# Kernel optimization log

Hardware: AMD Instinct MI355X
Metric: run time of the kernel (lower is better)

The kernel has to match this reference:

```python
import jax, jax.numpy as jnp
import numpy as np

PREF_DIM = 2
PREF_EMB = 64
HIDDEN = 512
NUM_CHUNKS = 105
CHUNK_EMB = 64
NUM_WS = 11
W_DIM = 20000


def setup_inputs() -> dict:
    key = jax.random.key(0)
    ks = jax.random.split(key, 12)
    in_dim = PREF_EMB + CHUNK_EMB
    inp = {
        "preference": jax.random.uniform(ks[0], (PREF_DIM,), dtype=jnp.float32),
        "pref_emb": 0.1 * jax.random.normal(ks[1], (PREF_DIM, PREF_EMB), dtype=jnp.float32),
        "chunk_emb": 0.1 * jax.random.normal(ks[2], (NUM_CHUNKS, CHUNK_EMB), dtype=jnp.float32),
        "W1": jax.random.normal(ks[3], (HIDDEN, in_dim), dtype=jnp.float32) / np.sqrt(in_dim),
        "b1": jnp.zeros((HIDDEN,), dtype=jnp.float32),
        "W2": jax.random.normal(ks[4], (HIDDEN, HIDDEN), dtype=jnp.float32) / np.sqrt(HIDDEN),
        "b2": jnp.zeros((HIDDEN,), dtype=jnp.float32),
        "W3": jax.random.normal(ks[5], (HIDDEN, HIDDEN), dtype=jnp.float32) / np.sqrt(HIDDEN),
        "b3": jnp.zeros((HIDDEN,), dtype=jnp.float32),
        "ws": 0.1 * jax.random.normal(ks[6], (NUM_WS, W_DIM, HIDDEN), dtype=jnp.float32),
    }
    return inp


def reference(preference, pref_emb, chunk_emb, W1, b1, W2, b2, W3, b3, ws):
    # pref_embedding = sum_i preference[i] * pref_emb[i]  -> [PREF_EMB]
    pref_embedding = preference @ pref_emb
    # Batch all chunks: concat(pref_embedding, chunk_emb[c]) -> [C, PREF_EMB+CHUNK_EMB]
    C = chunk_emb.shape[0]
    x = jnp.concatenate(
        [jnp.broadcast_to(pref_embedding, (C, pref_embedding.shape[0])), chunk_emb],
        axis=1,
    )
    # 3-layer MLP (Linear/ReLU/Linear/ReLU/Linear)
    h = jax.nn.relu(x @ W1.T + b1)
    h = jax.nn.relu(h @ W2.T + b2)
    rep = h @ W3.T + b3  # [C, HIDDEN]
    # Per chunk, concat over ws of F.linear(rep, w): [C, NUM_WS, W_DIM]
    out = jnp.einsum("ch,kwh->ckw", rep, ws)
    # Flat weight vector (original then reshapes contiguous slices into a dict;
    # that slicing is a pure view op on this vector)
    return out.reshape(-1)
```

## Files before the change

kernel.cpp:

```cpp
#include <hip/hip_runtime.h>


typedef __bf16 bf16x8 __attribute__((ext_vector_type(8)));
typedef float f32x4 __attribute__((ext_vector_type(4)));

#define NUM_CHUNKS 105
#define HIDDEN 512
#define N_COLS 220000
#define PAD_CHUNKS 112
#define REP_CHUNKS 7168

__global__ void mlp_kernel(const float* __restrict__ pref,
                           const float* __restrict__ pref_emb,
                           const float* __restrict__ chunk_emb,
                           const float* __restrict__ W1, const float* __restrict__ b1,
                           const float* __restrict__ W2, const float* __restrict__ b2,
                           const float* __restrict__ W3, const float* __restrict__ b3,
                           __bf16* __restrict__ repf) {
  __shared__ float x[128];
  __shared__ float h1[512];
  __shared__ float h2[512];
  const int tid = threadIdx.x;
  const int c = blockIdx.x;
  const int t = c >> 4, mmc = c & 15;

  if (c >= NUM_CHUNKS) {
    for (int jj = tid; jj < 512; jj += 256) {
      const int ss = jj >> 5, qq = (jj >> 3) & 3, j = jj & 7;
      const long idx = (((long)(ss * 7 + t) * 4 + qq) * 16 + mmc) * 8 + j;
      repf[idx] = (__bf16)0.f;
    }
    return;
  }

  if (tid < 64) {
    x[tid] = pref[0] * pref_emb[tid] + pref[1] * pref_emb[64 + tid];
  } else if (tid < 128) {
    x[tid] = chunk_emb[c * 64 + (tid - 64)];
  }
  __syncthreads();

  for (int jj = tid; jj < 512; jj += 256) {
    float s = b1[jj];
    const f32x4* wr = (const f32x4*)(W1 + jj * 128);
#pragma unroll
    for (int i = 0; i < 32; ++i) {
      f32x4 w = wr[i];
      s += w[0] * x[i * 4 + 0] + w[1] * x[i * 4 + 1] +
           w[2] * x[i * 4 + 2] + w[3] * x[i * 4 + 3];
    }
    h1[jj] = fmaxf(s, 0.f);
  }
  __syncthreads();

  for (int jj = tid; jj < 512; jj += 256) {
    float s = b2[jj];
    const f32x4* wr = (const f32x4*)(W2 + jj * 512);
#pragma unroll 8
    for (int i = 0; i < 128; ++i) {
      f32x4 w = wr[i];
      s += w[0] * h1[i * 4 + 0] + w[1] * h1[i * 4 + 1] +
           w[2] * h1[i * 4 + 2] + w[3] * h1[i * 4 + 3];
    }
    h2[jj] = fmaxf(s, 0.f);
  }
  __syncthreads();

  for (int jj = tid; jj < 512; jj += 256) {
    float s = b3[jj];
    const f32x4* wr = (const f32x4*)(W3 + jj * 512);
#pragma unroll 8
    for (int i = 0; i < 128; ++i) {
      f32x4 w = wr[i];
      s += w[0] * h2[i * 4 + 0] + w[1] * h2[i * 4 + 1] +
           w[2] * h2[i * 4 + 2] + w[3] * h2[i * 4 + 3];
    }
    const int ss = jj >> 5, qq = (jj >> 3) & 3, j = jj & 7;
    const long idx = (((long)(ss * 7 + t) * 4 + qq) * 16 + mmc) * 8 + j;
    repf[idx] = (__bf16)s;
  }
}

__global__ __launch_bounds__(256, 1) void gemm_ws(
    const float* __restrict__ ws,
    const bf16x8* __restrict__ repf,
    float* __restrict__ out) {
  __shared__ bf16x8 Alds[REP_CHUNKS];

  const int tid = threadIdx.x;
  const int lane = tid & 63;
  const int wv = tid >> 6;
  const int q = lane >> 4;
  const int mm = lane & 15;

#pragma unroll
  for (int i = 0; i < 28; ++i) {
    const bf16x8* g = repf + wv * 1792 + i * 64 + lane;
    __builtin_amdgcn_global_load_lds(
        (const __attribute__((address_space(1))) unsigned int*)g,
        (__attribute__((address_space(3))) unsigned int*)&Alds[wv * 1792 + i * 64],
        16, 0, 0);
  }

  const long cb = (long)blockIdx.x * 128 + wv * 32;
  const long col0 = cb + mm;
  const long col1 = col0 + 16;
  const bool v0 = col0 < N_COLS;
  const bool v1 = col1 < N_COLS;
  const long cl0 = v0 ? col0 : 0;
  const long cl1 = v1 ? col1 : 0;
  const f32x4* w0 = (const f32x4*)(ws + cl0 * 512) + q * 2;
  const f32x4* w1 = (const f32x4*)(ws + cl1 * 512) + q * 2;

  f32x4 X0[3], X1[3], Y0[3], Y1[3];
#pragma unroll
  for (int p = 0; p < 3; ++p) {
    X0[p] = __builtin_nontemporal_load(w0 + p * 8);
    X1[p] = __builtin_nontemporal_load(w0 + p * 8 + 1);
    Y0[p] = __builtin_nontemporal_load(w1 + p * 8);
    Y1[p] = __builtin_nontemporal_load(w1 + p * 8 + 1);
  }

  __syncthreads();

  f32x4 acc0[7], acc1[7];
#pragma unroll
  for (int t = 0; t < 7; ++t) {
    acc0[t] = (f32x4){0.f, 0.f, 0.f, 0.f};
    acc1[t] = (f32x4){0.f, 0.f, 0.f, 0.f};
  }

  bf16x8 Aa[7], Ab[7];
#pragma unroll
  for (int t = 0; t < 7; ++t) Aa[t] = Alds[t * 64 + lane];

#pragma unroll
  for (int s = 0; s < 16; ++s) {
    if (s < 15) {
#pragma unroll
      for (int t = 0; t < 7; ++t) {
        if (s & 1) Aa[t] = Alds[(s + 1) * 448 + t * 64 + lane];
        else       Ab[t] = Alds[(s + 1) * 448 + t * 64 + lane];
      }
    }
    const int slot = s % 3;
    f32x4 x0 = X0[slot], x1 = X1[slot], y0 = Y0[slot], y1 = Y1[slot];
    bf16x8 b0, b1;
#pragma unroll
    for (int j = 0; j < 4; ++j) {
      b0[j] = (__bf16)x0[j];
      b0[4 + j] = (__bf16)x1[j];
      b1[j] = (__bf16)y0[j];
      b1[4 + j] = (__bf16)y1[j];
    }
#pragma unroll
    for (int t = 0; t < 7; ++t) {
      bf16x8 a = (s & 1) ? Ab[t] : Aa[t];
      acc0[t] = __builtin_amdgcn_mfma_f32_16x16x32_bf16(a, b0, acc0[t], 0, 0, 0);
      acc1[t] = __builtin_amdgcn_mfma_f32_16x16x32_bf16(a, b1, acc1[t], 0, 0, 0);
    }
    if (s < 13) {
      X0[slot] = __builtin_nontemporal_load(w0 + (s + 3) * 8);
      X1[slot] = __builtin_nontemporal_load(w0 + (s + 3) * 8 + 1);
      Y0[slot] = __builtin_nontemporal_load(w1 + (s + 3) * 8);
      Y1[slot] = __builtin_nontemporal_load(w1 + (s + 3) * 8 + 1);
    }
  }

#pragma unroll
  for (int t = 0; t < 7; ++t) {
    const int mbase = t * 16 + q * 4;
#pragma unroll
    for (int r = 0; r < 4; ++r) {
      const int m = mbase + r;
      if (m < NUM_CHUNKS) {
        if (v0) __builtin_nontemporal_store(acc0[t][r], out + (long)m * N_COLS + col0);
        if (v1) __builtin_nontemporal_store(acc1[t][r], out + (long)m * N_COLS + col1);
      }
    }
  }
}

extern "C" void kernel_launch(void* const* d_in, const int* in_sizes, int n_in,
                              void* d_out, int out_size, void* d_ws, size_t ws_size,
                              hipStream_t stream) {
  const float* pref      = (const float*)d_in[0];
  const float* pref_emb  = (const float*)d_in[1];
  const float* chunk_emb = (const float*)d_in[2];
  const float* W1 = (const float*)d_in[3];
  const float* b1 = (const float*)d_in[4];
  const float* W2 = (const float*)d_in[5];
  const float* b2 = (const float*)d_in[6];
  const float* W3 = (const float*)d_in[7];
  const float* b3 = (const float*)d_in[8];
  const float* ws = (const float*)d_in[9];
  float* out = (float*)d_out;
  __bf16* repf = (__bf16*)d_ws;

  mlp_kernel<<<PAD_CHUNKS, 256, 0, stream>>>(pref, pref_emb, chunk_emb,
                                             W1, b1, W2, b2, W3, b3, repf);
  const int nblk = (N_COLS + 127) / 128;
  gemm_ws<<<nblk, 256, 0, stream>>>(ws, (const bf16x8*)d_ws, out);
}
```

Before: 719.6 us.

## Make ws GEMM persistent with cross-tile prefetch; widen MLP blocks to 512 threads

The ws GEMM becomes a persistent kernel of 256 blocks that loop over column tiles. The A operand is loaded into LDS once per block, and the first weight slices of the next tile are prefetched while the current tile finishes, with the prefetch depth raised from 3 to 4 stages. The MLP kernel runs with 512 threads so each thread computes one output, and it splits each dot product across four partial sums for more ILP. The goal is to amortise the LDS staging and launch tail and keep memory streaming across tiles. The risk is lower occupancy per CU and load imbalance across tiles.

```diff
diff --git a/kernel.cpp b/kernel.cpp
--- a/kernel.cpp
+++ b/kernel.cpp
@@ -9,6 +9,8 @@
 #define N_COLS 220000
 #define PAD_CHUNKS 112
 #define REP_CHUNKS 7168
+#define N_TILES 1719
+#define GEMM_BLOCKS 256
 
 __global__ void mlp_kernel(const float* __restrict__ pref,
                            const float* __restrict__ pref_emb,
@@ -23,13 +25,12 @@
   const int tid = threadIdx.x;
   const int c = blockIdx.x;
   const int t = c >> 4, mmc = c & 15;
+  const int jj = tid;
+  const int ss = jj >> 5, qq = (jj >> 3) & 3, j = jj & 7;
+  const long fidx = (((long)(ss * 7 + t) * 4 + qq) * 16 + mmc) * 8 + j;
 
   if (c >= NUM_CHUNKS) {
-    for (int jj = tid; jj < 512; jj += 256) {
-      const int ss = jj >> 5, qq = (jj >> 3) & 3, j = jj & 7;
-      const long idx = (((long)(ss * 7 + t) * 4 + qq) * 16 + mmc) * 8 + j;
-      repf[idx] = (__bf16)0.f;
-    }
+    repf[fidx] = (__bf16)0.f;
     return;
   }
 
@@ -40,44 +41,48 @@
   }
   __syncthreads();
 
-  for (int jj = tid; jj < 512; jj += 256) {
-    float s = b1[jj];
+  {
     const f32x4* wr = (const f32x4*)(W1 + jj * 128);
-#pragma unroll
-    for (int i = 0; i < 32; ++i) {
-      f32x4 w = wr[i];
-      s += w[0] * x[i * 4 + 0] + w[1] * x[i * 4 + 1] +
-           w[2] * x[i * 4 + 2] + w[3] * x[i * 4 + 3];
-    }
-    h1[jj] = fmaxf(s, 0.f);
-  }
-  __syncthreads();
-
-  for (int jj = tid; jj < 512; jj += 256) {
-    float s = b2[jj];
+    float p0 = 0.f, p1 = 0.f, p2 = 0.f, p3 = 0.f;
+#pragma unroll
+    for (int i = 0; i < 32; i += 4) {
+      f32x4 wa = wr[i], wb = wr[i + 1], wc = wr[i + 2], wd = wr[i + 3];
+      p0 += wa[0] * x[i * 4 + 0] + wa[1] * x[i * 4 + 1] + wa[2] * x[i * 4 + 2] + wa[3] * x[i * 4 + 3];
+      p1 += wb[0] * x[i * 4 + 4] + wb[1] * x[i * 4 + 5] + wb[2] * x[i * 4 + 6] + wb[3] * x[i * 4 + 7];
+      p2 += wc[0] * x[i * 4 + 8] + wc[1] * x[i * 4 + 9] + wc[2] * x[i * 4 + 10] + wc[3] * x[i * 4 + 11];
+      p3 += wd[0] * x[i * 4 + 12] + wd[1] * x[i * 4 + 13] + wd[2] * x[i * 4 + 14] + wd[3] * x[i * 4 + 15];
+    }
+    h1[jj] = fmaxf((p0 + p1) + (p2 + p3) + b1[jj], 0.f);
+  }
+  __syncthreads();
+
+  {
     const f32x4* wr = (const f32x4*)(W2 + jj * 512);
+    float p0 = 0.f, p1 = 0.f, p2 = 0.f, p3 = 0.f;
 #pragma unroll 8
-    for (int i = 0; i < 128; ++i) {
-      f32x4 w = wr[i];
-      s += w[0] * h1[i * 4 + 0] + w[1] * h1[i * 4 + 1] +
-           w[2] * h1[i * 4 + 2] + w[3] * h1[i * 4 + 3];
-    }
-    h2[jj] = fmaxf(s, 0.f);
-  }
-  __syncthreads();
-
-  for (int jj = tid; jj < 512; jj += 256) {
-    float s = b3[jj];
+    for (int i = 0; i < 128; i += 4) {
+      f32x4 wa = wr[i], wb = wr[i + 1], wc = wr[i + 2], wd = wr[i + 3];
+      p0 += wa[0] * h1[i * 4 + 0] + wa[1] * h1[i * 4 + 1] + wa[2] * h1[i * 4 + 2] + wa[3] * h1[i * 4 + 3];
+      p1 += wb[0] * h1[i * 4 + 4] + wb[1] * h1[i * 4 + 5] + wb[2] * h1[i * 4 + 6] + wb[3] * h1[i * 4 + 7];
+      p2 += wc[0] * h1[i * 4 + 8] + wc[1] * h1[i * 4 + 9] + wc[2] * h1[i * 4 + 10] + wc[3] * h1[i * 4 + 11];
+      p3 += wd[0] * h1[i * 4 + 12] + wd[1] * h1[i * 4 + 13] + wd[2] * h1[i * 4 + 14] + wd[3] * h1[i * 4 + 15];
+    }
+    h2[jj] = fmaxf((p0 + p1) + (p2 + p3) + b2[jj], 0.f);
+  }
+  __syncthreads();
+
+  {
     const f32x4* wr = (const f32x4*)(W3 + jj * 512);
+    float p0 = 0.f, p1 = 0.f, p2 = 0.f, p3 = 0.f;
 #pragma unroll 8
-    for (int i = 0; i < 128; ++i) {
-      f32x4 w = wr[i];
-      s += w[0] * h2[i * 4 + 0] + w[1] * h2[i * 4 + 1] +
-           w[2] * h2[i * 4 + 2] + w[3] * h2[i * 4 + 3];
-    }
-    const int ss = jj >> 5, qq = (jj >> 3) & 3, j = jj & 7;
-    const long idx = (((long)(ss * 7 + t) * 4 + qq) * 16 + mmc) * 8 + j;
-    repf[idx] = (__bf16)s;
+    for (int i = 0; i < 128; i += 4) {
+      f32x4 wa = wr[i], wb = wr[i + 1], wc = wr[i + 2], wd = wr[i + 3];
+      p0 += wa[0] * h2[i * 4 + 0] + wa[1] * h2[i * 4 + 1] + wa[2] * h2[i * 4 + 2] + wa[3] * h2[i * 4 + 3];
+      p1 += wb[0] * h2[i * 4 + 4] + wb[1] * h2[i * 4 + 5] + wb[2] * h2[i * 4 + 6] + wb[3] * h2[i * 4 + 7];
+      p2 += wc[0] * h2[i * 4 + 8] + wc[1] * h2[i * 4 + 9] + wc[2] * h2[i * 4 + 10] + wc[3] * h2[i * 4 + 11];
+      p3 += wd[0] * h2[i * 4 + 12] + wd[1] * h2[i * 4 + 13] + wd[2] * h2[i * 4 + 14] + wd[3] * h2[i * 4 + 15];
+    }
+    repf[fidx] = (__bf16)((p0 + p1) + (p2 + p3) + b3[jj]);
   }
 }
 
@@ -102,19 +107,18 @@
         16, 0, 0);
   }
 
-  const long cb = (long)blockIdx.x * 128 + wv * 32;
-  const long col0 = cb + mm;
-  const long col1 = col0 + 16;
-  const bool v0 = col0 < N_COLS;
-  const bool v1 = col1 < N_COLS;
-  const long cl0 = v0 ? col0 : 0;
-  const long cl1 = v1 ? col1 : 0;
-  const f32x4* w0 = (const f32x4*)(ws + cl0 * 512) + q * 2;
-  const f32x4* w1 = (const f32x4*)(ws + cl1 * 512) + q * 2;
-
-  f32x4 X0[3], X1[3], Y0[3], Y1[3];
-#pragma unroll
-  for (int p = 0; p < 3; ++p) {
+  long tile = blockIdx.x;
+  long cb = tile * 128 + wv * 32;
+  long col0 = cb + mm;
+  long col1 = col0 + 16;
+  bool v0 = col0 < N_COLS;
+  bool v1 = col1 < N_COLS;
+  const f32x4* w0 = (const f32x4*)(ws + (v0 ? col0 : 0) * 512) + q * 2;
+  const f32x4* w1 = (const f32x4*)(ws + (v1 ? col1 : 0) * 512) + q * 2;
+
+  f32x4 X0[4], X1[4], Y0[4], Y1[4];
+#pragma unroll
+  for (int p = 0; p < 4; ++p) {
     X0[p] = __builtin_nontemporal_load(w0 + p * 8);
     X1[p] = __builtin_nontemporal_load(w0 + p * 8 + 1);
     Y0[p] = __builtin_nontemporal_load(w1 + p * 8);
@@ -123,61 +127,83 @@
 
   __syncthreads();
 
-  f32x4 acc0[7], acc1[7];
-#pragma unroll
-  for (int t = 0; t < 7; ++t) {
-    acc0[t] = (f32x4){0.f, 0.f, 0.f, 0.f};
-    acc1[t] = (f32x4){0.f, 0.f, 0.f, 0.f};
-  }
-
   bf16x8 Aa[7], Ab[7];
 #pragma unroll
   for (int t = 0; t < 7; ++t) Aa[t] = Alds[t * 64 + lane];
 
-#pragma unroll
-  for (int s = 0; s < 16; ++s) {
-    if (s < 15) {
+  for (;;) {
+    f32x4 acc0[7], acc1[7];
+#pragma unroll
+    for (int t = 0; t < 7; ++t) {
+      acc0[t] = (f32x4){0.f, 0.f, 0.f, 0.f};
+      acc1[t] = (f32x4){0.f, 0.f, 0.f, 0.f};
+    }
+
+    const long ntile = tile + GEMM_BLOCKS;
+    const bool have_next = ntile < N_TILES;
+    long ncb = ntile * 128 + wv * 32;
+    long ncol0 = ncb + mm;
+    long ncol1 = ncol0 + 16;
+    bool nv0 = ncol0 < N_COLS;
+    bool nv1 = ncol1 < N_COLS;
+    const f32x4* nw0 = (const f32x4*)(ws + ((have_next && nv0) ? ncol0 : 0) * 512) + q * 2;
+    const f32x4* nw1 = (const f32x4*)(ws + ((have_next && nv1) ? ncol1 : 0) * 512) + q * 2;
+
+#pragma unroll
+    for (int s = 0; s < 16; ++s) {
+      const int slot = s & 3;
+      f32x4 x0 = X0[slot], x1 = X1[slot], y0 = Y0[slot], y1 = Y1[slot];
+      bf16x8 b0, b1;
+#pragma unroll
+      for (int jv = 0; jv < 4; ++jv) {
+        b0[jv] = (__bf16)x0[jv];
+        b0[4 + jv] = (__bf16)x1[jv];
+        b1[jv] = (__bf16)y0[jv];
+        b1[4 + jv] = (__bf16)y1[jv];
+      }
 #pragma unroll
       for (int t = 0; t < 7; ++t) {
-        if (s & 1) Aa[t] = Alds[(s + 1) * 448 + t * 64 + lane];
-        else       Ab[t] = Alds[(s + 1) * 448 + t * 64 + lane];
-      }
-    }
-    const int slot = s % 3;
-    f32x4 x0 = X0[slot], x1 = X1[slot], y0 = Y0[slot], y1 = Y1[slot];
-    bf16x8 b0, b1;
-#pragma unroll
-    for (int j = 0; j < 4; ++j) {
-      b0[j] = (__bf16)x0[j];
-      b0[4 + j] = (__bf16)x1[j];
-      b1[j] = (__bf16)y0[j];
-      b1[4 + j] = (__bf16)y1[j];
-    }
+        bf16x8 a = (s & 1) ? Ab[t] : Aa[t];
+        acc0[t] = __builtin_amdgcn_mfma_f32_16x16x32_bf16(a, b0, acc0[t], 0, 0, 0);
+        acc1[t] = __builtin_amdgcn_mfma_f32_16x16x32_bf16(a, b1, acc1[t], 0, 0, 0);
+      }
+      {
+        const int sn = (s + 1) & 15;
+#pragma unroll
+        for (int t = 0; t < 7; ++t) {
+          if (s & 1) Aa[t] = Alds[sn * 448 + t * 64 + lane];
+          else       Ab[t] = Alds[sn * 448 + t * 64 + lane];
+        }
+      }
+      if (s < 12) {
+        X0[slot] = __builtin_nontemporal_load(w0 + (s + 4) * 8);
+        X1[slot] = __builtin_nontemporal_load(w0 + (s + 4) * 8 + 1);
+        Y0[slot] = __builtin_nontemporal_load(w1 + (s + 4) * 8);
+        Y1[slot] = __builtin_nontemporal_load(w1 + (s + 4) * 8 + 1);
+      } else if (have_next) {
+        X0[slot] = __builtin_nontemporal_load(nw0 + (s - 12) * 8);
+        X1[slot] = __builtin_nontemporal_load(nw0 + (s - 12) * 8 + 1);
+        Y0[slot] = __builtin_nontemporal_load(nw1 + (s - 12) * 8);
+        Y1[slot] = __builtin_nontemporal_load(nw1 + (s - 12) * 8 + 1);
+      }
+    }
+
 #pragma unroll
     for (int t = 0; t < 7; ++t) {
-      bf16x8 a = (s & 1) ? Ab[t] : Aa[t];
-      acc0[t] = __builtin_amdgcn_mfma_f32_16x16x32_bf16(a, b0, acc0[t], 0, 0, 0);
-      acc1[t] = __builtin_amdgcn_mfma_f32_16x16x32_bf16(a, b1, acc1[t], 0, 0, 0);
-    }
-    if (s < 13) {
-      X0[slot] = __builtin_nontemporal_load(w0 + (s + 3) * 8);
-      X1[slot] = __builtin_nontemporal_load(w0 + (s + 3) * 8 + 1);
-      Y0[slot] = __builtin_nontemporal_load(w1 + (s + 3) * 8);
-      Y1[slot] = __builtin_nontemporal_load(w1 + (s + 3) * 8 + 1);
-    }
-  }
-
-#pragma unroll
-  for (int t = 0; t < 7; ++t) {
-    const int mbase = t * 16 + q * 4;
-#pragma unroll
-    for (int r = 0; r < 4; ++r) {
-      const int m = mbase + r;
-      if (m < NUM_CHUNKS) {
-        if (v0) __builtin_nontemporal_store(acc0[t][r], out + (long)m * N_COLS + col0);
-        if (v1) __builtin_nontemporal_store(acc1[t][r], out + (long)m * N_COLS + col1);
-      }
-    }
+      const int mbase = t * 16 + q * 4;
+#pragma unroll
+      for (int r = 0; r < 4; ++r) {
+        const int m = mbase + r;
+        if (m < NUM_CHUNKS) {
+          if (v0) __builtin_nontemporal_store(acc0[t][r], out + (long)m * N_COLS + col0);
+          if (v1) __builtin_nontemporal_store(acc1[t][r], out + (long)m * N_COLS + col1);
+        }
+      }
+    }
+
+    if (!have_next) break;
+    tile = ntile;
+    col0 = ncol0; col1 = ncol1; v0 = nv0; v1 = nv1; w0 = nw0; w1 = nw1;
   }
 }
 
@@ -197,8 +223,7 @@
   float* out = (float*)d_out;
   __bf16* repf = (__bf16*)d_ws;
 
-  mlp_kernel<<<PAD_CHUNKS, 256, 0, stream>>>(pref, pref_emb, chunk_emb,
+  mlp_kernel<<<PAD_CHUNKS, 512, 0, stream>>>(pref, pref_emb, chunk_emb,
                                              W1, b1, W2, b2, W3, b3, repf);
-  const int nblk = (N_COLS + 127) / 128;
-  gemm_ws<<<nblk, 256, 0, stream>>>(ws, (const bf16x8*)d_ws, out);
+  gemm_ws<<<GEMM_BLOCKS, 256, 0, stream>>>(ws, (const bf16x8*)d_ws, out);
 }
```

New measurement: 753.1 us. 1.05x slower.
